# Optimization experiments

Measured on AMD Instinct MI355X. Metric: run time of the kernel, lower is better.

The kernel has to match this reference:

```python
import jax, jax.numpy as jnp
import numpy as np

NUM_STEPS = 50
ALPHA = 0.1

def setup_inputs() -> dict:
    key = jax.random.key(0)
    initial_state = jax.random.normal(key, (8, 2048, 128), dtype=jnp.float32)
    return {"initial_state": initial_state}

def reference(initial_state):
    # Sequential 1D diffusion stencil with periodic (wraparound) boundary along axis 1.
    def step(s, _):
        s_next = s + ALPHA * (jnp.roll(s, 1, axis=1) + jnp.roll(s, -1, axis=1) - 2.0 * s)
        return s_next, s_next
    _, states = jax.lax.scan(step, initial_state, None, length=NUM_STEPS)
    # [num_steps+1, B, N, D]: initial state followed by each step's output
    return jnp.concatenate([initial_state[None], states], axis=0)
```

## Files before the change

kernel.cpp:

```cpp
#include <hip/hip_runtime.h>


namespace {

constexpr int   B      = 8;
constexpr int   N      = 2048;
constexpr int   D4     = 32;
constexpr int   STEPS  = 50;
constexpr float ALPHA  = 0.1f;
constexpr int   T      = 32;
constexpr int   HALO_L = 50;
constexpr int   R      = 136;
constexpr int   QG     = 8;
constexpr int   K      = R / QG;
constexpr int   CHUNKS = N / T;

__device__ __forceinline__ float4 stencil(const float4 p, const float4 c,
                                          const float4 n) {
    float4 r;
    r.x = c.x + ALPHA * (p.x + n.x - 2.0f * c.x);
    r.y = c.y + ALPHA * (p.y + n.y - 2.0f * c.y);
    r.z = c.z + ALPHA * (p.z + n.z - 2.0f * c.z);
    r.w = c.w + ALPHA * (p.w + n.w - 2.0f * c.w);
    return r;
}

__global__ __launch_bounds__(QG * D4) void diffusion_halo(
        const float4* __restrict__ in4, float4* __restrict__ out4) {
    const int tid = threadIdx.x;
    const int d4  = tid & (D4 - 1);
    const int q   = tid >> 5;
    const int b   = blockIdx.x / CHUNKS;
    const int n0  = (blockIdx.x % CHUNKS) * T;

    __shared__ float4 lo[2][QG][D4];
    __shared__ float4 hi[2][QG][D4];

    const int rbase = q * K;

    float4 s[K];
#pragma unroll
    for (int i = 0; i < K; ++i) {
        const int ng = (n0 + rbase + i + (N - HALO_L)) & (N - 1);
        s[i] = in4[(b * N + ng) * D4 + d4];
    }

#pragma unroll
    for (int i = 0; i < K; ++i) {
        const int r = rbase + i;
        if (r >= HALO_L && r < HALO_L + T) {
            out4[(b * N + (n0 + r - HALO_L)) * D4 + d4] = s[i];
        }
    }

    for (int k = 1; k <= STEPS; ++k) {
        const int buf = k & 1;
        lo[buf][q][d4] = s[0];
        hi[buf][q][d4] = s[K - 1];
        asm volatile("s_waitcnt lgkmcnt(0)" ::: "memory");
        __builtin_amdgcn_s_barrier();
        const float4 bl = (q > 0)      ? hi[buf][q - 1][d4]
                                       : make_float4(0.f, 0.f, 0.f, 0.f);
        const float4 bh = (q < QG - 1) ? lo[buf][q + 1][d4]
                                       : make_float4(0.f, 0.f, 0.f, 0.f);

        const int outbase = (k * B + b) * N;
        float4 prev = bl;
#pragma unroll
        for (int i = 0; i < K; ++i) {
            const float4 cur = s[i];
            float4 nxt = bh;
            if (i + 1 < K) nxt = s[i + 1];
            s[i] = stencil(prev, cur, nxt);
            prev = cur;
            const int r = rbase + i;
            if (r >= HALO_L && r < HALO_L + T) {
                out4[(outbase + (n0 + r - HALO_L)) * D4 + d4] = s[i];
            }
        }
    }
}

}

extern "C" void kernel_launch(void* const* d_in, const int* in_sizes, int n_in,
                              void* d_out, int out_size, void* d_ws, size_t ws_size,
                              hipStream_t stream) {
    const float4* in4  = reinterpret_cast<const float4*>(d_in[0]);
    float4*       out4 = reinterpret_cast<float4*>(d_out);

    dim3 grid(B * CHUNKS);
    dim3 block(QG * D4);
    diffusion_halo<<<grid, block, 0, stream>>>(in4, out4);
}
```

Measured before the change: 90.62 us.

## Split feature dim across blocks, shrink per-thread rows, use nontemporal stores

Splits the 32-float4 feature dimension into two halves handled by separate blocks, which doubles the grid to 1024 blocks. It also uses 16 row-groups of 9 rows each (144 rows, halo 56) in place of 8 groups of 17. Output stores become nontemporal to avoid polluting cache with the large write-only output. Fewer registers per thread should raise occupancy and parallelism, at the cost of more redundant halo computation and 16-float4-wide half-rows in memory accesses.

```diff
diff --git a/kernel.cpp b/kernel.cpp
--- a/kernel.cpp
+++ b/kernel.cpp
@@ -3,79 +3,82 @@
 
 namespace {
 
+typedef float f4 __attribute__((ext_vector_type(4)));
+
 constexpr int   B      = 8;
 constexpr int   N      = 2048;
 constexpr int   D4     = 32;
+constexpr int   SPLITD = 2;
+constexpr int   D4L    = D4 / SPLITD;
 constexpr int   STEPS  = 50;
 constexpr float ALPHA  = 0.1f;
 constexpr int   T      = 32;
-constexpr int   HALO_L = 50;
-constexpr int   R      = 136;
-constexpr int   QG     = 8;
-constexpr int   K      = R / QG;
+constexpr int   QG     = 16;
+constexpr int   K      = 9;
+constexpr int   R      = QG * K;
+constexpr int   HALO_L = (R - T) / 2;
 constexpr int   CHUNKS = N / T;
 
-__device__ __forceinline__ float4 stencil(const float4 p, const float4 c,
-                                          const float4 n) {
-    float4 r;
-    r.x = c.x + ALPHA * (p.x + n.x - 2.0f * c.x);
-    r.y = c.y + ALPHA * (p.y + n.y - 2.0f * c.y);
-    r.z = c.z + ALPHA * (p.z + n.z - 2.0f * c.z);
-    r.w = c.w + ALPHA * (p.w + n.w - 2.0f * c.w);
-    return r;
+__device__ __forceinline__ f4 stencil(const f4 p, const f4 c, const f4 n) {
+    return c + ALPHA * (p + n - 2.0f * c);
 }
 
-__global__ __launch_bounds__(QG * D4) void diffusion_halo(
-        const float4* __restrict__ in4, float4* __restrict__ out4) {
+__global__ __launch_bounds__(QG * D4L, 4) void diffusion_halo(
+        const f4* __restrict__ in4, f4* __restrict__ out4) {
     const int tid = threadIdx.x;
-    const int d4  = tid & (D4 - 1);
-    const int q   = tid >> 5;
-    const int b   = blockIdx.x / CHUNKS;
-    const int n0  = (blockIdx.x % CHUNKS) * T;
+    const int d4l = tid & (D4L - 1);
+    const int q   = tid >> 4;
 
-    __shared__ float4 lo[2][QG][D4];
-    __shared__ float4 hi[2][QG][D4];
+    const int bid = blockIdx.x;
+    const int dh  = bid & (SPLITD - 1);
+    const int c   = (bid >> 1) & (CHUNKS - 1);
+    const int b   = bid >> 7;
+    const int n0  = c * T;
+    const int d4g = dh * D4L + d4l;
+
+    __shared__ f4 lo[2][QG][D4L];
+    __shared__ f4 hi[2][QG][D4L];
 
     const int rbase = q * K;
 
-    float4 s[K];
+    f4 s[K];
 #pragma unroll
     for (int i = 0; i < K; ++i) {
         const int ng = (n0 + rbase + i + (N - HALO_L)) & (N - 1);
-        s[i] = in4[(b * N + ng) * D4 + d4];
+        s[i] = in4[(b * N + ng) * D4 + d4g];
     }
 
 #pragma unroll
     for (int i = 0; i < K; ++i) {
         const int r = rbase + i;
         if (r >= HALO_L && r < HALO_L + T) {
-            out4[(b * N + (n0 + r - HALO_L)) * D4 + d4] = s[i];
+            __builtin_nontemporal_store(
+                s[i], &out4[(b * N + (n0 + r - HALO_L)) * D4 + d4g]);
         }
     }
 
     for (int k = 1; k <= STEPS; ++k) {
         const int buf = k & 1;
-        lo[buf][q][d4] = s[0];
-        hi[buf][q][d4] = s[K - 1];
+        lo[buf][q][d4l] = s[0];
+        hi[buf][q][d4l] = s[K - 1];
         asm volatile("s_waitcnt lgkmcnt(0)" ::: "memory");
         __builtin_amdgcn_s_barrier();
-        const float4 bl = (q > 0)      ? hi[buf][q - 1][d4]
-                                       : make_float4(0.f, 0.f, 0.f, 0.f);
-        const float4 bh = (q < QG - 1) ? lo[buf][q + 1][d4]
-                                       : make_float4(0.f, 0.f, 0.f, 0.f);
+        const f4 bl = (q > 0)      ? hi[buf][q - 1][d4l] : (f4)(0.f);
+        const f4 bh = (q < QG - 1) ? lo[buf][q + 1][d4l] : (f4)(0.f);
 
         const int outbase = (k * B + b) * N;
-        float4 prev = bl;
+        f4 prev = bl;
 #pragma unroll
         for (int i = 0; i < K; ++i) {
-            const float4 cur = s[i];
-            float4 nxt = bh;
+            const f4 cur = s[i];
+            f4 nxt = bh;
             if (i + 1 < K) nxt = s[i + 1];
             s[i] = stencil(prev, cur, nxt);
             prev = cur;
             const int r = rbase + i;
             if (r >= HALO_L && r < HALO_L + T) {
-                out4[(outbase + (n0 + r - HALO_L)) * D4 + d4] = s[i];
+                __builtin_nontemporal_store(
+                    s[i], &out4[(outbase + (n0 + r - HALO_L)) * D4 + d4g]);
             }
         }
     }
@@ -86,10 +89,10 @@
 extern "C" void kernel_launch(void* const* d_in, const int* in_sizes, int n_in,
                               void* d_out, int out_size, void* d_ws, size_t ws_size,
                               hipStream_t stream) {
-    const float4* in4  = reinterpret_cast<const float4*>(d_in[0]);
-    float4*       out4 = reinterpret_cast<float4*>(d_out);
+    const f4* in4  = reinterpret_cast<const f4*>(d_in[0]);
+    f4*       out4 = reinterpret_cast<f4*>(d_out);
 
-    dim3 grid(B * CHUNKS);
-    dim3 block(QG * D4);
+    dim3 grid(B * CHUNKS * SPLITD);
+    dim3 block(QG * D4L);
     diffusion_halo<<<grid, block, 0, stream>>>(in4, out4);
 }
```

After: 89.93 us. No clear change (-0.8%).
